# Kernel tuning notes

Measured on AMD Instinct MI355X. Metric: run time of the kernel, lower is better.

## Reference

```python
import jax, jax.numpy as jnp
import numpy as np

L, B, N, D, H = 4, 4, 2048, 512, 8
HD = D // H  # head dim 64
EPS = 1e-5

def setup_inputs() -> dict:
    key = jax.random.key(0)
    ks = jax.random.split(key, 8)
    s = 0.02  # init scale for weights
    f32 = jnp.float32
    return {
        "x": jax.random.normal(ks[0], (B, N, D), f32),
        "Wq": jax.random.normal(ks[1], (L, D, D), f32) * s,
        "Wk": jax.random.normal(ks[2], (L, D, D), f32) * s,
        "Wv": jax.random.normal(ks[3], (L, D, D), f32) * s,
        "Wo": jax.random.normal(ks[4], (L, D, D), f32) * s,
        "bo": jnp.zeros((L, D), f32),
        "ln1_g": jnp.ones((L, D), f32),
        "ln1_b": jnp.zeros((L, D), f32),
        "W1": jax.random.normal(ks[5], (L, D, D), f32) * s,
        "b1": jnp.zeros((L, D), f32),
        "W2": jax.random.normal(ks[6], (L, D, D), f32) * s,
        "b2": jnp.zeros((L, D), f32),
        "ln2_g": jnp.ones((L, D), f32),
        "ln2_b": jnp.zeros((L, D), f32),
    }

def _layernorm(x, g, b):
    mu = jnp.mean(x, axis=-1, keepdims=True)
    var = jnp.mean(jnp.square(x - mu), axis=-1, keepdims=True)
    return (x - mu) * jax.lax.rsqrt(var + EPS) * g + b

def reference(x, Wq, Wk, Wv, Wo, bo, ln1_g, ln1_b, W1, b1, W2, b2, ln2_g, ln2_b):
    scale = D ** -0.5  # dim1 == dim on the cfg=None path

    def layer(h, p):
        wq, wk, wv, wo, bo_, g1, bb1, w1, bh1, w2, bh2, g2, bb2 = p
        # --- Residual(PreNorm(Attention)) ---
        y = _layernorm(h, g1, bb1)
        def split_heads(t):  # [B,N,D] -> [B,H,N,HD]
            return t.reshape(B, N, H, HD).transpose(0, 2, 1, 3)
        q = split_heads(y @ wq)
        k = split_heads(y @ wk)
        v = split_heads(y @ wv)
        dots = jnp.einsum('bhid,bhjd->bhij', q, k) * scale
        attn = jax.nn.softmax(dots, axis=-1)
        o = jnp.einsum('bhij,bhjd->bhid', attn, v)
        o = o.transpose(0, 2, 1, 3).reshape(B, N, D)
        h = h + o @ wo + bo_
        # --- Residual(PreNorm(FeedForward)) ---
        y = _layernorm(h, g2, bb2)
        y = jax.nn.gelu(y @ w1 + bh1, approximate=False)
        h = h + y @ w2 + bh2
        return h, None

    params = (Wq, Wk, Wv, Wo, bo, ln1_g, ln1_b, W1, b1, W2, b2, ln2_g, ln2_b)
    out, _ = jax.lax.scan(layer, x, params)
    return out
```

## Files before the change

kernel.cpp:

```cpp
#include <hip/hip_runtime.h>
#include <hip/hip_bf16.h>


typedef __bf16 bf16x8 __attribute__((ext_vector_type(8)));
typedef float f32x4 __attribute__((ext_vector_type(4)));
typedef unsigned int u32x4 __attribute__((ext_vector_type(4)));
typedef unsigned int u32x2 __attribute__((ext_vector_type(2)));
typedef unsigned short u16;

__device__ __forceinline__ u16 f2b(float f) {
  unsigned int u; __builtin_memcpy(&u, &f, 4);
  u += 0x7fffu + ((u >> 16) & 1u);
  return (u16)(u >> 16);
}
__device__ __forceinline__ bf16x8 ld8(const u16* p) {
  u32x4 t = *(const u32x4*)p;
  bf16x8 r; __builtin_memcpy(&r, &t, 16); return r;
}
__device__ __forceinline__ unsigned pkhi(float a, float b) {
  unsigned ua, ub; __builtin_memcpy(&ua, &a, 4); __builtin_memcpy(&ub, &b, 4);
  return __builtin_amdgcn_perm(ua, ub, 0x07060302u);
}

#define GLL(gp, lp) __builtin_amdgcn_global_load_lds( \
    (const __attribute__((address_space(1))) void*)(gp), \
    (__attribute__((address_space(3))) void*)(lp), 16, 0, 0)

__device__ __forceinline__ int swz(int r) { return (r + (r >> 2)) & 3; }

__global__ __launch_bounds__(256) void tr_all_k(
    const float* __restrict__ Wq, const float* __restrict__ Wk,
    const float* __restrict__ Wv, const float* __restrict__ Wo,
    const float* __restrict__ W1, const float* __restrict__ W2,
    u16* __restrict__ wtqkv, u16* __restrict__ wto,
    u16* __restrict__ wt1, u16* __restrict__ wt2) {
  __shared__ float t[32][33];
  int tx = threadIdx.x, ty = threadIdx.y;
  int z = blockIdx.z, which = z >> 2, l = z & 3;
  const float* in;
  u16* out;
  switch (which) {
    case 0: in = Wq; out = wtqkv + l * 786432; break;
    case 1: in = Wk; out = wtqkv + l * 786432 + 262144; break;
    case 2: in = Wv; out = wtqkv + l * 786432 + 524288; break;
    case 3: in = Wo; out = wto + l * 262144; break;
    case 4: in = W1; out = wt1 + l * 262144; break;
    default: in = W2; out = wt2 + l * 262144; break;
  }
  int k0 = blockIdx.y * 32, n0 = blockIdx.x * 32;
  const float* ip = in + l * 262144;
#pragma unroll
  for (int i = 0; i < 4; i++)
    t[ty + i * 8][tx] = ip[(k0 + ty + i * 8) * 512 + n0 + tx];
  __syncthreads();
#pragma unroll
  for (int i = 0; i < 4; i++)
    out[(n0 + ty + i * 8) * 512 + k0 + tx] = f2b(t[tx][ty + i * 8]);
}

__global__ __launch_bounds__(256) void ln_k(const float* __restrict__ h,
                                            const float* __restrict__ gg,
                                            const float* __restrict__ bb,
                                            u16* __restrict__ y) {
  int tid = threadIdx.x, wave = tid >> 6, lane = tid & 63;
  int tok = blockIdx.x * 4 + wave;
  const float* hp = h + (size_t)tok * 512 + lane * 8;
  float x[8];
  *(float4*)&x[0] = *(const float4*)hp;
  *(float4*)&x[4] = *(const float4*)(hp + 4);
  float s = 0.f, ss = 0.f;
#pragma unroll
  for (int i = 0; i < 8; i++) { s += x[i]; ss += x[i] * x[i]; }
#pragma unroll
  for (int off = 1; off < 64; off <<= 1) {
    s += __shfl_xor(s, off, 64);
    ss += __shfl_xor(ss, off, 64);
  }
  float mean = s * (1.0f / 512.0f);
  float var = ss * (1.0f / 512.0f) - mean * mean;
  float rstd = rsqrtf(var + 1e-5f);
  u32x4 ov;
#pragma unroll
  for (int i = 0; i < 4; i++) {
    int d0 = lane * 8 + i * 2;
    float y0 = (x[i * 2]     - mean) * rstd * gg[d0]     + bb[d0];
    float y1 = (x[i * 2 + 1] - mean) * rstd * gg[d0 + 1] + bb[d0 + 1];
    ov[i] = (unsigned)f2b(y0) | ((unsigned)f2b(y1) << 16);
  }
  *(u32x4*)&y[(size_t)tok * 512 + lane * 8] = ov;
}

enum { EPI_RES = 1, EPI_GELU = 2 };

template <int EPI>
__global__ __launch_bounds__(256, 4) void gemm2_k(
    const u16* __restrict__ A, const u16* __restrict__ Bt,
    const float* __restrict__ bias, u16* __restrict__ out0,
    const float* __restrict__ hin, float* __restrict__ hout,
    float* __restrict__ fout) {
  __shared__ __align__(16) u16 As[2][64 * 32];
  __shared__ __align__(16) u16 Bs[2][128 * 32];
  const int tid = threadIdx.x;
  const int wave = tid >> 6, lane = tid & 63;
  const int quad = lane >> 4, l16 = lane & 15;
  const int wm = wave >> 1, wn = wave & 1;
  const int m0 = blockIdx.x * 64;
  const int n0 = blockIdx.y * 128;
  const int mb = m0 + wm * 32, nb = n0 + wn * 64;

  float hr[2][4][4];
  if constexpr (EPI == EPI_RES) {
#pragma unroll
    for (int mi = 0; mi < 2; ++mi)
#pragma unroll
      for (int ni = 0; ni < 4; ++ni) {
        int r0 = mb + mi * 16 + quad * 4, c = nb + ni * 16 + l16;
#pragma unroll
        for (int g = 0; g < 4; ++g)
          hr[mi][ni][g] = hin[(size_t)(r0 + g) * 512 + c];
      }
  }

  f32x4 acc[2][4];
#pragma unroll
  for (int i = 0; i < 2; i++)
#pragma unroll
    for (int j = 0; j < 4; j++) acc[i][j] = f32x4{0.f, 0.f, 0.f, 0.f};

  const int sA0 = wave * 64 + lane;
  const int rowA = sA0 >> 2, cgA = (sA0 & 3) ^ swz(rowA);
  const size_t agl = (size_t)(m0 + rowA) * 512 + cgA * 8;
  int rowB[2], cgB[2];
#pragma unroll
  for (int rnd = 0; rnd < 2; ++rnd) {
    int s = rnd * 256 + sA0;
    rowB[rnd] = s >> 2;
    cgB[rnd] = (s & 3) ^ swz(rowB[rnd]);
  }
  const size_t bgl0 = (size_t)(n0 + rowB[0]) * 512 + cgB[0] * 8;
  const size_t bgl1 = (size_t)(n0 + rowB[1]) * 512 + cgB[1] * 8;

  int kbA[2], kbB[4];
#pragma unroll
  for (int mi = 0; mi < 2; ++mi) {
    int r = wm * 32 + mi * 16 + l16;
    kbA[mi] = r * 32 + (quad ^ swz(r)) * 8;
  }
#pragma unroll
  for (int ni = 0; ni < 4; ++ni) {
    int r = wn * 64 + ni * 16 + l16;
    kbB[ni] = r * 32 + (quad ^ swz(r)) * 8;
  }

  GLL(A + agl, &As[0][(wave * 64) * 8]);
  GLL(Bt + bgl0, &Bs[0][(wave * 64) * 8]);
  GLL(Bt + bgl1, &Bs[0][(256 + wave * 64) * 8]);

#pragma unroll 2
  for (int kt = 0; kt < 16; ++kt) {
    __syncthreads();
    const u16* AsB = As[kt & 1];
    const u16* BsB = Bs[kt & 1];
    if (kt + 1 < 16) {
      u16* AsN = (u16*)As[(kt & 1) ^ 1];
      u16* BsN = (u16*)Bs[(kt & 1) ^ 1];
      const int k1 = (kt + 1) * 32;
      GLL(A + agl + k1, AsN + (wave * 64) * 8);
      GLL(Bt + bgl0 + k1, BsN + (wave * 64) * 8);
      GLL(Bt + bgl1 + k1, BsN + (256 + wave * 64) * 8);
    }

    bf16x8 af[2], bf_[4];
#pragma unroll
    for (int mi = 0; mi < 2; ++mi) af[mi] = ld8(AsB + kbA[mi]);
#pragma unroll
    for (int ni = 0; ni < 4; ++ni) bf_[ni] = ld8(BsB + kbB[ni]);
#pragma unroll
    for (int mi = 0; mi < 2; ++mi)
#pragma unroll
      for (int ni = 0; ni < 4; ++ni)
        acc[mi][ni] = __builtin_amdgcn_mfma_f32_16x16x32_bf16(
            af[mi], bf_[ni], acc[mi][ni], 0, 0, 0);
  }

#pragma unroll
  for (int mi = 0; mi < 2; ++mi) {
#pragma unroll
    for (int ni = 0; ni < 4; ++ni) {
      f32x4 a = acc[mi][ni];
      int r0 = mb + mi * 16 + quad * 4;
      int c = nb + ni * 16 + l16;
      float bi = bias[c];
      if constexpr (EPI == EPI_RES) {
#pragma unroll
        for (int g = 0; g < 4; ++g) {
          float v = hr[mi][ni][g] + a[g] + bi;
          hout[(size_t)(r0 + g) * 512 + c] = v;
          if (fout) fout[(size_t)(r0 + g) * 512 + c] = v;
        }
      } else {
#pragma unroll
        for (int g = 0; g < 4; ++g) {
          float t = a[g] + bi;
          float gl = 0.5f * t * (1.0f + erff(t * 0.70710678118654752f));
          out0[(size_t)(r0 + g) * 512 + c] = f2b(gl);
        }
      }
    }
  }
}

__global__ __launch_bounds__(256, 4) void gemm_qkv_k(
    const u16* __restrict__ A, const u16* __restrict__ Bt,
    u16* __restrict__ outq, u16* __restrict__ outk, u16* __restrict__ outvt) {
  __shared__ __align__(16) u16 As[2][128 * 32];
  __shared__ __align__(16) u16 Bs[2][128 * 32];
  const int tid = threadIdx.x;
  const int wave = tid >> 6, lane = tid & 63;
  const int quad = lane >> 4, l16 = lane & 15;
  const int wm = wave >> 1, wn = wave & 1;
  const int m0 = blockIdx.x * 128;
  const int n0 = blockIdx.y * 128;

  f32x4 acc[4][4];
#pragma unroll
  for (int i = 0; i < 4; i++)
#pragma unroll
    for (int j = 0; j < 4; j++) acc[i][j] = f32x4{0.f, 0.f, 0.f, 0.f};

  const int sA0 = wave * 64 + lane;
  size_t agl[2], bgl[2];
#pragma unroll
  for (int rnd = 0; rnd < 2; ++rnd) {
    int s = rnd * 256 + sA0;
    int row = s >> 2, cg = (s & 3) ^ swz(row);
    agl[rnd] = (size_t)(m0 + row) * 512 + cg * 8;
    bgl[rnd] = (size_t)(n0 + row) * 512 + cg * 8;
  }

  int kbA[4], kbB[4];
#pragma unroll
  for (int mi = 0; mi < 4; ++mi) {
    int r = wm * 64 + mi * 16 + l16;
    kbA[mi] = r * 32 + (quad ^ swz(r)) * 8;
  }
#pragma unroll
  for (int ni = 0; ni < 4; ++ni) {
    int r = wn * 64 + ni * 16 + l16;
    kbB[ni] = r * 32 + (quad ^ swz(r)) * 8;
  }

  GLL(A + agl[0], &As[0][(wave * 64) * 8]);
  GLL(A + agl[1], &As[0][(256 + wave * 64) * 8]);
  GLL(Bt + bgl[0], &Bs[0][(wave * 64) * 8]);
  GLL(Bt + bgl[1], &Bs[0][(256 + wave * 64) * 8]);

#pragma unroll 2
  for (int kt = 0; kt < 16; ++kt) {
    __syncthreads();
    const u16* AsB = As[kt & 1];
    const u16* BsB = Bs[kt & 1];
    if (kt + 1 < 16) {
      u16* AsN = (u16*)As[(kt & 1) ^ 1];
      u16* BsN = (u16*)Bs[(kt & 1) ^ 1];
      const int k1 = (kt + 1) * 32;
      GLL(A + agl[0] + k1, AsN + (wave * 64) * 8);
      GLL(A + agl[1] + k1, AsN + (256 + wave * 64) * 8);
      GLL(Bt + bgl[0] + k1, BsN + (wave * 64) * 8);
      GLL(Bt + bgl[1] + k1, BsN + (256 + wave * 64) * 8);
    }

    bf16x8 af[4], bf_[4];
#pragma unroll
    for (int mi = 0; mi < 4; ++mi) af[mi] = ld8(AsB + kbA[mi]);
#pragma unroll
    for (int ni = 0; ni < 4; ++ni) bf_[ni] = ld8(BsB + kbB[ni]);
#pragma unroll
    for (int mi = 0; mi < 4; ++mi)
#pragma unroll
      for (int ni = 0; ni < 4; ++ni)
        acc[mi][ni] = __builtin_amdgcn_mfma_f32_16x16x32_bf16(
            af[mi], bf_[ni], acc[mi][ni], 0, 0, 0);
  }

  const int mb = m0 + wm * 64, nb = n0 + wn * 64;
#pragma unroll
  for (int mi = 0; mi < 4; ++mi) {
#pragma unroll
    for (int ni = 0; ni < 4; ++ni) {
      f32x4 a = acc[mi][ni];
      int r0 = mb + mi * 16 + quad * 4;
      int c = nb + ni * 16 + l16;
      if (c < 512) {
        const float C2 = 0.06375871506958306f;
#pragma unroll
        for (int g = 0; g < 4; ++g) outq[(size_t)(r0 + g) * 512 + c] = f2b(a[g] * C2);
      } else if (c < 1024) {
#pragma unroll
        for (int g = 0; g < 4; ++g) outk[(size_t)(r0 + g) * 512 + (c - 512)] = f2b(a[g]);
      } else {
        int cv = c - 1024, hh = cv >> 6, dd = cv & 63;
        int bb = r0 >> 11, nt = r0 & 2047;
        u32x2 pk;
        pk[0] = (unsigned)f2b(a[0]) | ((unsigned)f2b(a[1]) << 16);
        pk[1] = (unsigned)f2b(a[2]) | ((unsigned)f2b(a[3]) << 16);
        *(u32x2*)&outvt[((size_t)(bb * 8 + hh) * 64 + dd) * 2048 + nt] = pk;
      }
    }
  }
}

__global__ __launch_bounds__(256, 4) void attn_k(const u16* __restrict__ q,
                                                 const u16* __restrict__ k,
                                                 const u16* __restrict__ vt,
                                                 u16* __restrict__ o) {
  __shared__ __align__(16) u16 Ks[2][64 * 64];
  __shared__ __align__(16) u16 Vs[2][64 * 64];
  __shared__ float Lr[4][32];
  const int tid = threadIdx.x, wave = tid >> 6, lane = tid & 63;
  const int quad = lane >> 4, l16 = lane & 15;
  const int swl = l16 & 7;
  const int qh2 = wave & 1, kvs = wave >> 1;
  const int bh = blockIdx.x, b = bh >> 3, h = bh & 7;
  const int qt0 = blockIdx.y * 64;

  const u16* qpb = q + (size_t)(b * 2048 + qt0 + qh2 * 32) * 512 + h * 64;
  bf16x8 aq[2][2];
#pragma unroll
  for (int qt = 0; qt < 2; ++qt) {
    const u16* qp = qpb + (size_t)(qt * 16 + l16) * 512;
    aq[qt][0] = ld8(qp + quad * 8);
    aq[qt][1] = ld8(qp + 32 + quad * 8);
  }

  const u16* kp = k + (size_t)b * 2048 * 512 + h * 64;
  const u16* vp = vt + (size_t)bh * 64 * 2048;

  const int srow = lane >> 3, schk = lane & 7, sgc = schk ^ srow;
  const int krow0 = wave * 8 + srow;
  const size_t kgl0 = (size_t)krow0 * 512 + sgc * 8;
  const size_t kgl1 = (size_t)(krow0 + 32) * 512 + sgc * 8;
  const size_t vgl0 = (size_t)krow0 * 2048 + sgc * 8;
  const size_t vgl1 = (size_t)(krow0 + 32) * 2048 + sgc * 8;

  int kb[2][2];
#pragma unroll
  for (int t = 0; t < 2; ++t) {
    kb[t][0] = (kvs * 32 + t * 16 + l16) * 64 + ((quad)     ^ swl) * 8;
    kb[t][1] = (kvs * 32 + t * 16 + l16) * 64 + ((4 + quad) ^ swl) * 8;
  }
  const int vblo = l16 * 64 + (((kvs << 2) + (quad >> 1)) ^ swl) * 8 + (quad & 1) * 4;
  const int vbhi = l16 * 64 + (((kvs << 2) + 2 + (quad >> 1)) ^ swl) * 8 + (quad & 1) * 4;

  f32x4 oacc[4][2];
#pragma unroll
  for (int i = 0; i < 4; i++)
#pragma unroll
    for (int j = 0; j < 2; j++) oacc[i][j] = f32x4{0.f, 0.f, 0.f, 0.f};
  f32x4 lsacc[2];
  lsacc[0] = f32x4{0.f, 0.f, 0.f, 0.f};
  lsacc[1] = f32x4{0.f, 0.f, 0.f, 0.f};

  u32x4 onesw;
  onesw[0] = 0x3F803F80u; onesw[1] = 0x3F803F80u;
  onesw[2] = 0x3F803F80u; onesw[3] = 0x3F803F80u;
  bf16x8 onesf; __builtin_memcpy(&onesf, &onesw, 16);

  GLL(kp + kgl0, &Ks[0][(wave * 8) * 64]);
  GLL(kp + kgl1, &Ks[0][(32 + wave * 8) * 64]);
  GLL(vp + vgl0, &Vs[0][(wave * 8) * 64]);
  GLL(vp + vgl1, &Vs[0][(32 + wave * 8) * 64]);

#pragma unroll 2
  for (int kt = 0; kt < 32; ++kt) {
    __syncthreads();
    const u16* KsB = Ks[kt & 1];
    const u16* VsB = Vs[kt & 1];
    if (kt + 1 < 32) {
      u16* KsN = (u16*)Ks[(kt & 1) ^ 1];
      u16* VsN = (u16*)Vs[(kt & 1) ^ 1];
      const u16* kpn = kp + (size_t)(kt + 1) * 32768;
      const u16* vpn = vp + (size_t)(kt + 1) * 64;
      GLL(kpn + kgl0, KsN + (wave * 8) * 64);
      GLL(kpn + kgl1, KsN + (32 + wave * 8) * 64);
      GLL(vpn + vgl0, VsN + (wave * 8) * 64);
      GLL(vpn + vgl1, VsN + (32 + wave * 8) * 64);
    }

    bf16x8 kf[2][2];
#pragma unroll
    for (int t = 0; t < 2; ++t) {
      kf[t][0] = ld8(KsB + kb[t][0]);
      kf[t][1] = ld8(KsB + kb[t][1]);
    }
    f32x4 sa[2][2];
    __builtin_amdgcn_s_setprio(1);
#pragma unroll
    for (int t = 0; t < 2; ++t)
#pragma unroll
      for (int qt = 0; qt < 2; ++qt) {
        f32x4 z = f32x4{0.f, 0.f, 0.f, 0.f};
        z = __builtin_amdgcn_mfma_f32_16x16x32_bf16(kf[t][0], aq[qt][0], z, 0, 0, 0);
        z = __builtin_amdgcn_mfma_f32_16x16x32_bf16(kf[t][1], aq[qt][1], z, 0, 0, 0);
        sa[t][qt] = z;
      }
    __builtin_amdgcn_s_setprio(0);

    u32x4 pw[2];
#pragma unroll
    for (int t = 0; t < 2; ++t)
#pragma unroll
      for (int qt = 0; qt < 2; ++qt) {
        float p0 = __builtin_amdgcn_exp2f(sa[t][qt][0]);
        float p1 = __builtin_amdgcn_exp2f(sa[t][qt][1]);
        float p2 = __builtin_amdgcn_exp2f(sa[t][qt][2]);
        float p3 = __builtin_amdgcn_exp2f(sa[t][qt][3]);
        pw[qt][t * 2]     = pkhi(p1, p0);
        pw[qt][t * 2 + 1] = pkhi(p3, p2);
      }
    bf16x8 pf[2];
    __builtin_memcpy(&pf[0], &pw[0], 16);
    __builtin_memcpy(&pf[1], &pw[1], 16);

    __builtin_amdgcn_s_setprio(1);
#pragma unroll
    for (int dt = 0; dt < 4; ++dt) {
      u32x2 lo = *(const u32x2*)(VsB + vblo + dt * 1024);
      u32x2 hi = *(const u32x2*)(VsB + vbhi + dt * 1024);
      u32x4 w;
      w[0] = lo[0]; w[1] = lo[1]; w[2] = hi[0]; w[3] = hi[1];
      bf16x8 av; __builtin_memcpy(&av, &w, 16);
#pragma unroll
      for (int qt = 0; qt < 2; ++qt)
        oacc[dt][qt] = __builtin_amdgcn_mfma_f32_16x16x32_bf16(
            av, pf[qt], oacc[dt][qt], 0, 0, 0);
    }
#pragma unroll
    for (int qt = 0; qt < 2; ++qt)
      lsacc[qt] = __builtin_amdgcn_mfma_f32_16x16x32_bf16(
          onesf, pf[qt], lsacc[qt], 0, 0, 0);
    __builtin_amdgcn_s_setprio(0);
  }

  if (quad == 0) {
#pragma unroll
    for (int qt = 0; qt < 2; ++qt) Lr[wave][qt * 16 + l16] = lsacc[qt][0];
  }
  __syncthreads();

  float* R = (float*)&Ks[0][0];
  const int l7 = lane & 7;
  if (wave >= 2) {
    float* Rw = R + (wave - 2) * 2048;
#pragma unroll
    for (int dt = 0; dt < 4; ++dt)
#pragma unroll
      for (int qt = 0; qt < 2; ++qt) {
        int s = (dt * 2 + qt) ^ l7;
        *(f32x4*)&Rw[lane * 32 + s * 4] = oacc[dt][qt];
      }
  }
  __syncthreads();
  if (wave < 2) {
    float* Rw = R + wave * 2048;
    float inv[2];
#pragma unroll
    for (int qt = 0; qt < 2; ++qt)
      inv[qt] = 1.0f / (Lr[wave][qt * 16 + l16] + Lr[wave + 2][qt * 16 + l16]);
#pragma unroll
    for (int dt = 0; dt < 4; ++dt)
#pragma unroll
      for (int qt = 0; qt < 2; ++qt) {
        int s = (dt * 2 + qt) ^ l7;
        f32x4 v = *(f32x4*)&Rw[lane * 32 + s * 4];
        float i4 = inv[qt];
        float o0 = (oacc[dt][qt][0] + v[0]) * i4;
        float o1 = (oacc[dt][qt][1] + v[1]) * i4;
        float o2 = (oacc[dt][qt][2] + v[2]) * i4;
        float o3 = (oacc[dt][qt][3] + v[3]) * i4;
        u16* op = o + (size_t)(b * 2048 + qt0 + wave * 32 + qt * 16 + l16) * 512 +
                  h * 64 + dt * 16 + quad * 4;
        u32x2 pk;
        pk[0] = (unsigned)f2b(o0) | ((unsigned)f2b(o1) << 16);
        pk[1] = (unsigned)f2b(o2) | ((unsigned)f2b(o3) << 16);
        *(u32x2*)op = pk;
      }
  }
}

extern "C" void kernel_launch(void* const* d_in, const int* in_sizes, int n_in,
                              void* d_out, int out_size, void* d_ws,
                              size_t ws_size, hipStream_t stream) {
  const float* x   = (const float*)d_in[0];
  const float* Wq  = (const float*)d_in[1];
  const float* Wk  = (const float*)d_in[2];
  const float* Wv  = (const float*)d_in[3];
  const float* Wo  = (const float*)d_in[4];
  const float* bo  = (const float*)d_in[5];
  const float* g1  = (const float*)d_in[6];
  const float* bg1 = (const float*)d_in[7];
  const float* W1  = (const float*)d_in[8];
  const float* b1  = (const float*)d_in[9];
  const float* W2  = (const float*)d_in[10];
  const float* b2  = (const float*)d_in[11];
  const float* g2  = (const float*)d_in[12];
  const float* bg2 = (const float*)d_in[13];

  char* ws = (char*)d_ws;
  float* h    = (float*)ws;
  u16* yb     = (u16*)(ws + (16ll << 20));
  u16* qb     = (u16*)(ws + (24ll << 20));
  u16* kb     = (u16*)(ws + (32ll << 20));
  u16* vtb    = (u16*)(ws + (40ll << 20));
  u16* ob     = (u16*)(ws + (48ll << 20));
  u16* wtqkv  = (u16*)(ws + (56ll << 20));
  u16* wto    = (u16*)(ws + (62ll << 20));
  u16* wt1    = (u16*)(ws + (64ll << 20));
  u16* wt2    = (u16*)(ws + (66ll << 20));

  tr_all_k<<<dim3(16, 16, 24), dim3(32, 8), 0, stream>>>(
      Wq, Wk, Wv, Wo, W1, W2, wtqkv, wto, wt1, wt2);

  for (int l = 0; l < 4; ++l) {
    const float* hsrc = (l == 0) ? x : h;
    ln_k<<<2048, 256, 0, stream>>>(hsrc, g1 + l * 512, bg1 + l * 512, yb);
    gemm_qkv_k<<<dim3(64, 12), 256, 0, stream>>>(
        yb, wtqkv + l * 786432, qb, kb, vtb);
    attn_k<<<dim3(32, 32), 256, 0, stream>>>(qb, kb, vtb, ob);
    gemm2_k<EPI_RES><<<dim3(128, 4), 256, 0, stream>>>(
        ob, wto + l * 262144, bo + l * 512, nullptr, hsrc, h, nullptr);
    ln_k<<<2048, 256, 0, stream>>>(h, g2 + l * 512, bg2 + l * 512, yb);
    gemm2_k<EPI_GELU><<<dim3(128, 4), 256, 0, stream>>>(
        yb, wt1 + l * 262144, b1 + l * 512, qb, nullptr, nullptr, nullptr);
    gemm2_k<EPI_RES><<<dim3(128, 4), 256, 0, stream>>>(
        qb, wt2 + l * 262144, b2 + l * 512, nullptr, h, h,
        (l == 3) ? (float*)d_out : nullptr);
  }
}
```

Measured before the change: 587.5 us.

## Triple-buffer K/V tiles in attention with explicit vmcnt waits

```diff
diff --git a/kernel.cpp b/kernel.cpp
--- a/kernel.cpp
+++ b/kernel.cpp
@@ -310,12 +310,11 @@
   }
 }
 
-__global__ __launch_bounds__(256, 4) void attn_k(const u16* __restrict__ q,
+__global__ __launch_bounds__(256, 3) void attn_k(const u16* __restrict__ q,
                                                  const u16* __restrict__ k,
                                                  const u16* __restrict__ vt,
                                                  u16* __restrict__ o) {
-  __shared__ __align__(16) u16 Ks[2][64 * 64];
-  __shared__ __align__(16) u16 Vs[2][64 * 64];
+  __shared__ __align__(16) u16 S[3 * 4096 * 2];
   __shared__ float Lr[4][32];
   const int tid = threadIdx.x, wave = tid >> 6, lane = tid & 63;
   const int quad = lane >> 4, l16 = lane & 15;
@@ -366,25 +365,40 @@
   onesw[2] = 0x3F803F80u; onesw[3] = 0x3F803F80u;
   bf16x8 onesf; __builtin_memcpy(&onesf, &onesw, 16);
 
-  GLL(kp + kgl0, &Ks[0][(wave * 8) * 64]);
-  GLL(kp + kgl1, &Ks[0][(32 + wave * 8) * 64]);
-  GLL(vp + vgl0, &Vs[0][(wave * 8) * 64]);
-  GLL(vp + vgl1, &Vs[0][(32 + wave * 8) * 64]);
-
-#pragma unroll 2
+  u16* Kb = S;
+  u16* Vb = S + 12288;
+  const int dst0 = (wave * 8) * 64, dst1 = (32 + wave * 8) * 64;
+
+  GLL(kp + kgl0, Kb + dst0);
+  GLL(kp + kgl1, Kb + dst1);
+  GLL(vp + vgl0, Vb + dst0);
+  GLL(vp + vgl1, Vb + dst1);
+  GLL(kp + 32768 + kgl0, Kb + 4096 + dst0);
+  GLL(kp + 32768 + kgl1, Kb + 4096 + dst1);
+  GLL(vp + 64 + vgl0, Vb + 4096 + dst0);
+  GLL(vp + 64 + vgl1, Vb + 4096 + dst1);
+
+  int ofA = 0, ofB = 4096, ofC = 8192;
+
   for (int kt = 0; kt < 32; ++kt) {
-    __syncthreads();
-    const u16* KsB = Ks[kt & 1];
-    const u16* VsB = Vs[kt & 1];
-    if (kt + 1 < 32) {
-      u16* KsN = (u16*)Ks[(kt & 1) ^ 1];
-      u16* VsN = (u16*)Vs[(kt & 1) ^ 1];
-      const u16* kpn = kp + (size_t)(kt + 1) * 32768;
-      const u16* vpn = vp + (size_t)(kt + 1) * 64;
-      GLL(kpn + kgl0, KsN + (wave * 8) * 64);
-      GLL(kpn + kgl1, KsN + (32 + wave * 8) * 64);
-      GLL(vpn + vgl0, VsN + (wave * 8) * 64);
-      GLL(vpn + vgl1, VsN + (32 + wave * 8) * 64);
+    if (kt < 31) {
+      asm volatile("s_waitcnt vmcnt(4)" ::: "memory");
+    } else {
+      asm volatile("s_waitcnt vmcnt(0)" ::: "memory");
+    }
+    __builtin_amdgcn_sched_barrier(0);
+    __builtin_amdgcn_s_barrier();
+    __builtin_amdgcn_sched_barrier(0);
+
+    const u16* KsB = Kb + ofA;
+    const u16* VsB = Vb + ofA;
+    if (kt + 2 < 32) {
+      const u16* kpn = kp + (size_t)(kt + 2) * 32768;
+      const u16* vpn = vp + (size_t)(kt + 2) * 64;
+      GLL(kpn + kgl0, Kb + ofC + dst0);
+      GLL(kpn + kgl1, Kb + ofC + dst1);
+      GLL(vpn + vgl0, Vb + ofC + dst0);
+      GLL(vpn + vgl1, Vb + ofC + dst1);
     }
 
     bf16x8 kf[2][2];
@@ -440,6 +454,8 @@
       lsacc[qt] = __builtin_amdgcn_mfma_f32_16x16x32_bf16(
           onesf, pf[qt], lsacc[qt], 0, 0, 0);
     __builtin_amdgcn_s_setprio(0);
+
+    int tmp = ofA; ofA = ofB; ofB = ofC; ofC = tmp;
   }
 
   if (quad == 0) {
@@ -448,7 +464,7 @@
   }
   __syncthreads();
 
-  float* R = (float*)&Ks[0][0];
+  float* R = (float*)S;
   const int l7 = lane & 7;
   if (wave >= 2) {
     float* Rw = R + (wave - 2) * 2048;
```

New measurement: 615.2 us. 1.05x slower.
